# Optimization experiments

Hardware: AMD Instinct MI355X
Metric: run time of the kernel (lower is better)

The kernel has to match this reference:

```python
import jax, jax.numpy as jnp
import numpy as np

P = 512
B = 256
D = P - 1          # 511
H = P * 10         # 5120


def setup_inputs() -> dict:
    key = jax.random.key(0)
    ks = jax.random.split(key, 12)
    theta_12 = jax.random.normal(ks[0], (B, D), dtype=jnp.float32)
    s_12 = jax.random.normal(ks[1], (B, D), dtype=jnp.float32)
    w_12 = jax.random.normal(ks[2], (B, D), dtype=jnp.float32)
    # make inv_Theta_11 symmetric positive definite so sqrt(quad_prod) is valid
    A = jax.random.normal(ks[3], (B, D, D), dtype=jnp.float32)
    inv_Theta_11 = jnp.einsum('bik,bjk->bij', A, A) / D + jnp.eye(D, dtype=jnp.float32)[None]
    Theta = jax.random.normal(ks[4], (B, P, P), dtype=jnp.float32)
    # phi_learner params: Linear(D, H) -> ReLU -> Linear(H, D)
    phi_w1 = jax.random.normal(ks[5], (H, D), dtype=jnp.float32) / np.sqrt(D)
    phi_b1 = jnp.zeros((H,), dtype=jnp.float32)
    phi_w2 = jax.random.normal(ks[6], (D, H), dtype=jnp.float32) / np.sqrt(H)
    phi_b2 = jnp.zeros((D,), dtype=jnp.float32)
    # st_param_learner params: Linear(1, 5) -> ReLU -> Linear(5, 1) -> Abs
    st_w1 = jax.random.normal(ks[7], (5, 1), dtype=jnp.float32)
    st_b1 = jax.random.normal(ks[8], (5,), dtype=jnp.float32) * 0.1
    st_w2 = jax.random.normal(ks[9], (1, 5), dtype=jnp.float32)
    st_b2 = jax.random.normal(ks[10], (1,), dtype=jnp.float32) * 0.1
    return dict(theta_12=theta_12, s_12=s_12, w_12=w_12, inv_Theta_11=inv_Theta_11,
                Theta=Theta, col=0,
                phi_w1=phi_w1, phi_b1=phi_b1, phi_w2=phi_w2, phi_b2=phi_b2,
                st_w1=st_w1, st_b1=st_b1, st_w2=st_w2, st_b2=st_b2)


def reference(theta_12, s_12, w_12, inv_Theta_11, Theta, col,
              phi_w1, phi_b1, phi_w2, phi_b2, st_w1, st_b1, st_w2, st_b2):
    # phi_learner: Linear -> ReLU -> Linear
    h = jax.nn.relu(theta_12 @ phi_w1.T + phi_b1)          # [B, H]
    phi = h @ phi_w2.T + phi_b2                            # [B, D]
    # batched quadratic form: phi @ inv_Theta_11 @ phi
    quad = jnp.einsum('bi,bij,bj->b', phi, inv_Theta_11, phi)[:, None]  # [B, 1]
    zeta = jnp.float32(1.0)
    phi_n = phi * jnp.sqrt(zeta) / jnp.sqrt(quad)          # [B, D]
    # st_param_learner applied elementwise (Linear(1,5)->ReLU->Linear(5,1)->Abs)
    x = phi_n[..., None]                                   # [B, D, 1]
    g = jax.nn.relu(x * st_w1[None, None, :, 0] + st_b1)   # [B, D, 5]
    lam = jnp.abs(g @ st_w2[0] + st_b2[0])                 # [B, D]
    Lambda = lam * 0.1
    return jnp.sign(phi_n) * jnp.maximum(0.0, jnp.abs(phi_n) - Lambda)
```

## Files before the change

kernel.cpp:

```cpp
#include <hip/hip_runtime.h>
#include <hip/hip_bf16.h>

#define B_ 256
#define D_ 511
#define H_ 5120
#define NTOT (D_ * D_)

typedef __attribute__((ext_vector_type(4))) float floatx4;
typedef __attribute__((ext_vector_type(8))) short short8;

union I4S8 { int4 i4; short8 s8; };

__device__ __forceinline__ unsigned short f2bf(float v) {
    __hip_bfloat16 h = __float2bfloat16(v);
    return __builtin_bit_cast(unsigned short, h);
}

__device__ __forceinline__ int sw_off(int row, int chunk) {
    return row * 128 + ((chunk ^ (row & 7)) * 16);
}

__global__ __launch_bounds__(256) void gemm1_mfma(
    const float* __restrict__ A, const float* __restrict__ W,
    const float* __restrict__ bias, __hip_bfloat16* __restrict__ Hout)
{
    __shared__ char lds[16384];
    char* Ab = lds;
    char* Bb = lds + 8192;
    const int t = threadIdx.x;
    const int m0 = blockIdx.y * 64;
    const int n0 = blockIdx.x * 64;
    const int lane = t & 63, wave = t >> 6;
    const int wm = (wave & 1) * 32, wn = (wave >> 1) * 32;
    const int lrow = lane & 15, lq = lane >> 4;

    floatx4 acc[2][2] = {};

    const int srow = t >> 6;
    const int sk   = t & 63;

    for (int k0 = 0; k0 < 512; k0 += 64) {
        __syncthreads();
        const bool kv = (k0 + sk) < D_;
        const int wroff = (((sk >> 3) ^ 0) * 0); (void)wroff;
        #pragma unroll
        for (int r = 0; r < 64; r += 4) {
            int row = r + srow;
            float av = kv ? A[(size_t)(m0 + row) * D_ + k0 + sk] : 0.f;
            float bv = kv ? W[(size_t)(n0 + row) * D_ + k0 + sk] : 0.f;
            int off = row * 128 + (((sk >> 3) ^ (row & 7)) * 16) + (sk & 7) * 2;
            *(unsigned short*)(Ab + off) = f2bf(av);
            *(unsigned short*)(Bb + off) = f2bf(bv);
        }
        __syncthreads();
        #pragma unroll
        for (int ks = 0; ks < 2; ++ks) {
            int kc = ks * 4 + lq;
            I4S8 af[2], bf[2];
            #pragma unroll
            for (int i = 0; i < 2; ++i) {
                af[i].i4 = *(const int4*)(Ab + sw_off(wm + i * 16 + lrow, kc));
                bf[i].i4 = *(const int4*)(Bb + sw_off(wn + i * 16 + lrow, kc));
            }
            #pragma unroll
            for (int i = 0; i < 2; ++i)
                #pragma unroll
                for (int j = 0; j < 2; ++j)
                    acc[i][j] = __builtin_amdgcn_mfma_f32_16x16x32_bf16(
                        af[i].s8, bf[j].s8, acc[i][j], 0, 0, 0);
        }
    }

    #pragma unroll
    for (int i = 0; i < 2; ++i) {
        #pragma unroll
        for (int j = 0; j < 2; ++j) {
            int n = n0 + wn + j * 16 + lrow;
            float bsv = bias[n];
            #pragma unroll
            for (int r = 0; r < 4; ++r) {
                int m = m0 + wm + i * 16 + lq * 4 + r;
                float v = acc[i][j][r] + bsv;
                v = v > 0.f ? v : 0.f;
                Hout[(size_t)m * H_ + n] = __float2bfloat16(v);
            }
        }
    }
}

__global__ __launch_bounds__(256) void gemm2_mfma(
    const __hip_bfloat16* __restrict__ Hm, const float* __restrict__ W,
    float* __restrict__ phi)
{
    __shared__ char lds[16384];
    char* Ab = lds;
    char* Bb = lds + 8192;
    const int t = threadIdx.x;
    const int n0 = blockIdx.x * 64;
    const int m0 = blockIdx.y * 64;
    const int kbeg = blockIdx.z * 640;
    const int lane = t & 63, wave = t >> 6;
    const int wm = (wave & 1) * 32, wn = (wave >> 1) * 32;
    const int lrow = lane & 15, lq = lane >> 4;

    floatx4 acc[2][2] = {};

    const int ra_ = t >> 3;
    const int ca_ = t & 7;
    const int rw_ = t >> 4;
    const int f4_ = t & 15;

    for (int k0 = 0; k0 < 640; k0 += 64) {
        __syncthreads();
        #pragma unroll
        for (int q = 0; q < 2; ++q) {
            int row = ra_ + 32 * q;
            int4 raw = *(const int4*)(Hm + (size_t)(m0 + row) * H_ + kbeg + k0 + ca_ * 8);
            *(int4*)(Ab + sw_off(row, ca_)) = raw;
        }
        #pragma unroll
        for (int q = 0; q < 4; ++q) {
            int row = rw_ + 16 * q;
            int n = n0 + row;
            float4 fv = make_float4(0.f, 0.f, 0.f, 0.f);
            if (n < D_) fv = *(const float4*)(W + (size_t)n * H_ + kbeg + k0 + f4_ * 4);
            unsigned int lo = (unsigned)f2bf(fv.x) | ((unsigned)f2bf(fv.y) << 16);
            unsigned int hi = (unsigned)f2bf(fv.z) | ((unsigned)f2bf(fv.w) << 16);
            int2 w8; w8.x = (int)lo; w8.y = (int)hi;
            int off = row * 128 + ((((f4_ >> 1) ^ (row & 7))) * 16) + (f4_ & 1) * 8;
            *(int2*)(Bb + off) = w8;
        }
        __syncthreads();
        #pragma unroll
        for (int ks = 0; ks < 2; ++ks) {
            int kc = ks * 4 + lq;
            I4S8 af[2], bf[2];
            #pragma unroll
            for (int i = 0; i < 2; ++i) {
                af[i].i4 = *(const int4*)(Ab + sw_off(wm + i * 16 + lrow, kc));
                bf[i].i4 = *(const int4*)(Bb + sw_off(wn + i * 16 + lrow, kc));
            }
            #pragma unroll
            for (int i = 0; i < 2; ++i)
                #pragma unroll
                for (int j = 0; j < 2; ++j)
                    acc[i][j] = __builtin_amdgcn_mfma_f32_16x16x32_bf16(
                        af[i].s8, bf[j].s8, acc[i][j], 0, 0, 0);
        }
    }

    #pragma unroll
    for (int i = 0; i < 2; ++i) {
        #pragma unroll
        for (int j = 0; j < 2; ++j) {
            int n = n0 + wn + j * 16 + lrow;
            if (n < D_) {
                #pragma unroll
                for (int r = 0; r < 4; ++r) {
                    int m = m0 + wm + i * 16 + lq * 4 + r;
                    atomicAdd(&phi[(size_t)m * D_ + n], acc[i][j][r]);
                }
            }
        }
    }
}

__global__ __launch_bounds__(512) void quad_final(
    const float* __restrict__ Mmat, const float* __restrict__ b2,
    const float* __restrict__ stw1, const float* __restrict__ stb1,
    const float* __restrict__ stw2, const float* __restrict__ stb2,
    float* __restrict__ phi_out)
{
    __shared__ float p[D_ + 1];
    __shared__ float red[8];
    __shared__ float qsh;
    const int b = blockIdx.x;
    const int t = threadIdx.x;

    if (t < D_) p[t] = phi_out[(size_t)b * D_ + t] + b2[t];
    __syncthreads();

    const size_t base = (size_t)b * NTOT;
    const float* Mb = Mmat + base;
    const int a0 = (int)((4 - (base & 3)) & 3);
    float acc = 0.f;

    if (t < a0) {
        int f = t;
        int r = f / D_; int c = f - r * D_;
        acc += Mb[f] * p[r] * p[c];
    }
    const int nvec = (NTOT - a0) >> 2;
    for (int v = t; v < nvec; v += 512) {
        int f = a0 + v * 4;
        float4 mv = *(const float4*)(Mb + f);
        int f0 = f,     r0 = f0 / D_, c0 = f0 - r0 * D_;
        int f1 = f + 1, r1 = f1 / D_, c1 = f1 - r1 * D_;
        int f2 = f + 2, r2 = f2 / D_, c2 = f2 - r2 * D_;
        int f3 = f + 3, r3 = f3 / D_, c3 = f3 - r3 * D_;
        acc += mv.x * (p[r0] * p[c0]);
        acc += mv.y * (p[r1] * p[c1]);
        acc += mv.z * (p[r2] * p[c2]);
        acc += mv.w * (p[r3] * p[c3]);
    }
    const int tbeg = a0 + nvec * 4;
    if (t < NTOT - tbeg) {
        int f = tbeg + t;
        int r = f / D_; int c = f - r * D_;
        acc += Mb[f] * p[r] * p[c];
    }

    #pragma unroll
    for (int off = 32; off > 0; off >>= 1) acc += __shfl_down(acc, off, 64);
    if ((t & 63) == 0) red[t >> 6] = acc;
    __syncthreads();
    if (t == 0) {
        float s = 0.f;
        #pragma unroll
        for (int w = 0; w < 8; ++w) s += red[w];
        qsh = s;
    }
    __syncthreads();

    const float q = qsh;
    if (t < D_) {
        float x = p[t] / sqrtf(q);
        float lam = stb2[0];
        #pragma unroll
        for (int k = 0; k < 5; ++k) {
            float g = x * stw1[k] + stb1[k];
            g = g > 0.f ? g : 0.f;
            lam += g * stw2[k];
        }
        lam = fabsf(lam) * 0.1f;
        float ax = fabsf(x) - lam;
        ax = ax > 0.f ? ax : 0.f;
        float s = (x > 0.f) ? 1.f : ((x < 0.f) ? -1.f : 0.f);
        phi_out[(size_t)b * D_ + t] = s * ax;
    }
}

extern "C" void kernel_launch(void* const* d_in, const int* in_sizes, int n_in,
                              void* d_out, int out_size, void* d_ws, size_t ws_size,
                              hipStream_t stream)
{
    const float* theta = (const float*)d_in[0];
    const float* invT  = (const float*)d_in[3];
    const float* w1    = (const float*)d_in[6];
    const float* b1    = (const float*)d_in[7];
    const float* w2    = (const float*)d_in[8];
    const float* b2    = (const float*)d_in[9];
    const float* stw1  = (const float*)d_in[10];
    const float* stb1  = (const float*)d_in[11];
    const float* stw2  = (const float*)d_in[12];
    const float* stb2  = (const float*)d_in[13];
    float* out = (float*)d_out;

    __hip_bfloat16* h = (__hip_bfloat16*)d_ws;

    hipMemsetAsync(out, 0, (size_t)B_ * D_ * sizeof(float), stream);

    gemm1_mfma<<<dim3(80, 4), 256, 0, stream>>>(theta, w1, b1, h);

    gemm2_mfma<<<dim3(8, 4, 8), 256, 0, stream>>>(h, w2, out);

    quad_final<<<B_, 512, 0, stream>>>(invT, b2, stw1, stb1, stw2, stb2, out);
}
```

Baseline: 554.8 us.

## Replace split-K atomics with partial buffers and row-wise quad form

The split-K GEMM2 now writes per-slice partial results to a workspace buffer instead of using atomicAdd, and the final kernel sums the eight partials. This also removes the memset of the output. The quadratic-form kernel is restructured so each wave handles whole rows with float4 loads, which avoids per-element integer division to recover row and column indices, and it uses 1024 threads per block. The cost is extra workspace traffic for the partials and alignment handling on every row.

```diff
diff --git a/kernel.cpp b/kernel.cpp
--- a/kernel.cpp
+++ b/kernel.cpp
@@ -42,7 +42,6 @@
     for (int k0 = 0; k0 < 512; k0 += 64) {
         __syncthreads();
         const bool kv = (k0 + sk) < D_;
-        const int wroff = (((sk >> 3) ^ 0) * 0); (void)wroff;
         #pragma unroll
         for (int r = 0; r < 64; r += 4) {
             int row = r + srow;
@@ -90,7 +89,7 @@
 
 __global__ __launch_bounds__(256) void gemm2_mfma(
     const __hip_bfloat16* __restrict__ Hm, const float* __restrict__ W,
-    float* __restrict__ phi)
+    float* __restrict__ part)
 {
     __shared__ char lds[16384];
     char* Ab = lds;
@@ -149,6 +148,7 @@
         }
     }
 
+    float* Cp = part + (size_t)blockIdx.z * (B_ * D_);
     #pragma unroll
     for (int i = 0; i < 2; ++i) {
         #pragma unroll
@@ -158,72 +158,70 @@
                 #pragma unroll
                 for (int r = 0; r < 4; ++r) {
                     int m = m0 + wm + i * 16 + lq * 4 + r;
-                    atomicAdd(&phi[(size_t)m * D_ + n], acc[i][j][r]);
+                    Cp[(size_t)m * D_ + n] = acc[i][j][r];
                 }
             }
         }
     }
 }
 
-__global__ __launch_bounds__(512) void quad_final(
-    const float* __restrict__ Mmat, const float* __restrict__ b2,
+__global__ __launch_bounds__(1024) void quad_final(
+    const float* __restrict__ Mmat, const float* __restrict__ part,
+    const float* __restrict__ b2,
     const float* __restrict__ stw1, const float* __restrict__ stb1,
     const float* __restrict__ stw2, const float* __restrict__ stb2,
-    float* __restrict__ phi_out)
-{
-    __shared__ float p[D_ + 1];
-    __shared__ float red[8];
+    float* __restrict__ out)
+{
+    __shared__ float p[512];
+    __shared__ float red[16];
     __shared__ float qsh;
     const int b = blockIdx.x;
     const int t = threadIdx.x;
-
-    if (t < D_) p[t] = phi_out[(size_t)b * D_ + t] + b2[t];
+    const int lane = t & 63, wv = t >> 6;
+
+    if (t < D_) {
+        float s = b2[t];
+        #pragma unroll
+        for (int z = 0; z < 8; ++z)
+            s += part[(size_t)z * (B_ * D_) + (size_t)b * D_ + t];
+        p[t] = s;
+    }
     __syncthreads();
 
-    const size_t base = (size_t)b * NTOT;
-    const float* Mb = Mmat + base;
-    const int a0 = (int)((4 - (base & 3)) & 3);
+    const float* Mb = Mmat + (size_t)b * NTOT;
     float acc = 0.f;
 
-    if (t < a0) {
-        int f = t;
-        int r = f / D_; int c = f - r * D_;
-        acc += Mb[f] * p[r] * p[c];
-    }
-    const int nvec = (NTOT - a0) >> 2;
-    for (int v = t; v < nvec; v += 512) {
-        int f = a0 + v * 4;
-        float4 mv = *(const float4*)(Mb + f);
-        int f0 = f,     r0 = f0 / D_, c0 = f0 - r0 * D_;
-        int f1 = f + 1, r1 = f1 / D_, c1 = f1 - r1 * D_;
-        int f2 = f + 2, r2 = f2 / D_, c2 = f2 - r2 * D_;
-        int f3 = f + 3, r3 = f3 / D_, c3 = f3 - r3 * D_;
-        acc += mv.x * (p[r0] * p[c0]);
-        acc += mv.y * (p[r1] * p[c1]);
-        acc += mv.z * (p[r2] * p[c2]);
-        acc += mv.w * (p[r3] * p[c3]);
-    }
-    const int tbeg = a0 + nvec * 4;
-    if (t < NTOT - tbeg) {
-        int f = tbeg + t;
-        int r = f / D_; int c = f - r * D_;
-        acc += Mb[f] * p[r] * p[c];
+    for (int i = wv; i < D_; i += 16) {
+        const float* row = Mb + (size_t)i * D_;
+        const int mis = (b + 3 * i) & 3;
+        const int headN = (4 - mis) & 3;
+        const int nv = (D_ - headN) >> 2;
+        float s = 0.f;
+        if (lane < headN) s += row[lane] * p[lane];
+        for (int v = lane; v < nv; v += 64) {
+            int c = headN + v * 4;
+            float4 m4 = *(const float4*)(row + c);
+            s += m4.x * p[c] + m4.y * p[c + 1] + m4.z * p[c + 2] + m4.w * p[c + 3];
+        }
+        int tb = headN + (nv << 2);
+        if (lane < D_ - tb) s += row[tb + lane] * p[tb + lane];
+        acc += s * p[i];
     }
 
     #pragma unroll
     for (int off = 32; off > 0; off >>= 1) acc += __shfl_down(acc, off, 64);
-    if ((t & 63) == 0) red[t >> 6] = acc;
+    if (lane == 0) red[wv] = acc;
     __syncthreads();
     if (t == 0) {
         float s = 0.f;
         #pragma unroll
-        for (int w = 0; w < 8; ++w) s += red[w];
+        for (int w = 0; w < 16; ++w) s += red[w];
         qsh = s;
     }
     __syncthreads();
 
-    const float q = qsh;
     if (t < D_) {
+        const float q = qsh;
         float x = p[t] / sqrtf(q);
         float lam = stb2[0];
         #pragma unroll
@@ -235,8 +233,8 @@
         lam = fabsf(lam) * 0.1f;
         float ax = fabsf(x) - lam;
         ax = ax > 0.f ? ax : 0.f;
-        float s = (x > 0.f) ? 1.f : ((x < 0.f) ? -1.f : 0.f);
-        phi_out[(size_t)b * D_ + t] = s * ax;
+        float sgn = (x > 0.f) ? 1.f : ((x < 0.f) ? -1.f : 0.f);
+        out[(size_t)b * D_ + t] = sgn * ax;
     }
 }
 
@@ -257,12 +255,11 @@
     float* out = (float*)d_out;
 
     __hip_bfloat16* h = (__hip_bfloat16*)d_ws;
-
-    hipMemsetAsync(out, 0, (size_t)B_ * D_ * sizeof(float), stream);
+    float* part = (float*)((char*)d_ws + (size_t)B_ * H_ * 2);
 
     gemm1_mfma<<<dim3(80, 4), 256, 0, stream>>>(theta, w1, b1, h);
 
-    gemm2_mfma<<<dim3(8, 4, 8), 256, 0, stream>>>(h, w2, out);
-
-    quad_final<<<B_, 512, 0, stream>>>(invT, b2, stw1, stb1, stw2, stb2, out);
-}
+    gemm2_mfma<<<dim3(8, 4, 8), 256, 0, stream>>>(h, w2, part);
+
+    quad_final<<<B_, 1024, 0, stream>>>(invT, part, b2, stw1, stb1, stw2, stb2, out);
+}
```

After: 558.1 us. Within noise of the previous version (+0.6%).
